# Performance work log

Hardware: AMD Instinct MI355X
Metric: run time of the kernel (lower is better)

The kernel has to match this reference:

```python
import jax, jax.numpy as jnp
import numpy as np

B, S, D, H = 32, 512, 1024, 16
DH = D // H
EPS = 1e-5
NEG = -1e9


def layer_norm(x, g, b):
    mu = jnp.mean(x, axis=-1, keepdims=True)
    var = jnp.mean(jnp.square(x - mu), axis=-1, keepdims=True)
    return (x - mu) * jax.lax.rsqrt(var + EPS) * g + b


def setup_inputs() -> dict:
    key = jax.random.key(0)
    ks = jax.random.split(key, 12)
    s = 1.0 / np.sqrt(D)
    inp = {
        "qk": jax.random.normal(ks[0], (B, S, D), jnp.float32),
        "v": jax.random.normal(ks[1], (B, S, D), jnp.float32),
        "mask": jax.random.randint(ks[2], (B, S), 0, 2).astype(jnp.int32),
        "qk_ln_g": jnp.ones((D,), jnp.float32),
        "qk_ln_b": jnp.zeros((D,), jnp.float32),
        "v_ln_g": jnp.ones((D,), jnp.float32),
        "v_ln_b": jnp.zeros((D,), jnp.float32),
        "Wq": jax.random.normal(ks[3], (D, D), jnp.float32) * s,
        "bq": jnp.zeros((D,), jnp.float32),
        "Wk": jax.random.normal(ks[4], (D, D), jnp.float32) * s,
        "bk": jnp.zeros((D,), jnp.float32),
        "Wv": jax.random.normal(ks[5], (D, D), jnp.float32) * s,
        "bv": jnp.zeros((D,), jnp.float32),
        "Wo": jax.random.normal(ks[6], (D, D), jnp.float32) * s,
        "bo": jnp.zeros((D,), jnp.float32),
    }
    return inp


def reference(qk, v, mask, qk_ln_g, qk_ln_b, v_ln_g, v_ln_b,
              Wq, bq, Wk, bk, Wv, bv, Wo, bo):
    # dual pre-norm
    qk_n = layer_norm(qk, qk_ln_g, qk_ln_b)          # [B,S,D]
    v_n = layer_norm(v, v_ln_g, v_ln_b)              # [B,S,D]
    # projections -> [B,S,H,DH]
    q = (qk_n @ Wq + bq).reshape(B, S, H, DH)
    k = (qk_n @ Wk + bk).reshape(B, S, H, DH)
    vv = (v_n @ Wv + bv).reshape(B, S, H, DH)
    # attention scores with key-padding mask
    scores = jnp.einsum("bqhd,bkhd->bhqk", q, k) / np.sqrt(DH)
    scores = jnp.where(mask[:, None, None, :] == 0, NEG, scores)
    attn = jax.nn.softmax(scores, axis=-1)           # [B,H,Sq,Sk]
    ctx = jnp.einsum("bhqk,bkhd->bqhd", attn, vv).reshape(B, S, D)
    a = ctx @ Wo + bo                                # output projection
    # residual on the normalized v (dropout is identity at eval)
    return v_n + a
```

## Files before the change

### kernel.cpp

```cpp
#include <hip/hip_runtime.h>
#include <hip/hip_bf16.h>

typedef __bf16 bf16;
typedef __bf16 bf16x2 __attribute__((ext_vector_type(2)));
typedef __bf16 bf16x4 __attribute__((ext_vector_type(4)));
typedef __bf16 bf16x8 __attribute__((ext_vector_type(8)));
typedef float f32x4 __attribute__((ext_vector_type(4)));

#define B_ 32
#define S_ 512
#define D_ 1024
#define H_ 16
#define DH_ 64
#define M_ (B_*S_)

#if __has_builtin(__builtin_amdgcn_exp2f)
#define FEXP2 __builtin_amdgcn_exp2f
#else
#define FEXP2 exp2f
#endif

__device__ __forceinline__ void async16(const void* g, void* l) {
  __builtin_amdgcn_global_load_lds(
      (const __attribute__((address_space(1))) unsigned int*)g,
      (__attribute__((address_space(3))) unsigned int*)l, 16, 0, 0);
}

__global__ __launch_bounds__(256) void ln_bf16(
    const float* __restrict__ qk, const float* __restrict__ v,
    const float* __restrict__ g1, const float* __restrict__ b1,
    const float* __restrict__ g2, const float* __restrict__ b2,
    bf16* __restrict__ o1, bf16* __restrict__ o2)
{
  int row = blockIdx.x;
  const float* src; const float* g; const float* b; bf16* o; int r;
  if (row < M_) { src=qk; g=g1; b=b1; o=o1; r=row; }
  else          { src=v;  g=g2; b=b2; o=o2; r=row-M_; }
  int t = threadIdx.x;
  float4 x = ((const float4*)(src + (size_t)r*D_))[t];
  float s  = x.x+x.y+x.z+x.w;
  float ss = x.x*x.x + x.y*x.y + x.z*x.z + x.w*x.w;
  #pragma unroll
  for (int off=32; off>=1; off>>=1) {
    s  += __shfl_xor(s,  off, 64);
    ss += __shfl_xor(ss, off, 64);
  }
  __shared__ float red[8];
  int w = t>>6, l = t&63;
  if (l==0){ red[w]=s; red[4+w]=ss; }
  __syncthreads();
  s  = red[0]+red[1]+red[2]+red[3];
  ss = red[4]+red[5]+red[6]+red[7];
  float mu  = s*(1.f/D_);
  float var = ss*(1.f/D_) - mu*mu;
  float rs  = rsqrtf(var + 1e-5f);
  float4 gg = ((const float4*)g)[t];
  float4 bb = ((const float4*)b)[t];
  bf16x4 ov;
  ov[0] = (bf16)((x.x-mu)*rs*gg.x + bb.x);
  ov[1] = (bf16)((x.y-mu)*rs*gg.y + bb.y);
  ov[2] = (bf16)((x.z-mu)*rs*gg.z + bb.z);
  ov[3] = (bf16)((x.w-mu)*rs*gg.w + bb.w);
  ((bf16x4*)(o + (size_t)r*D_))[t] = ov;
}

__global__ void wtrans(const float* __restrict__ W0, const float* __restrict__ W1,
                       const float* __restrict__ W2, const float* __restrict__ W3,
                       bf16* __restrict__ o0, bf16* __restrict__ o1,
                       bf16* __restrict__ o2, bf16* __restrict__ o3)
{
  int z = blockIdx.z;
  const float* W = z==0?W0: z==1?W1: z==2?W2: W3;
  bf16* o        = z==0?o0: z==1?o1: z==2?o2: o3;
  __shared__ float tile[32][33];
  int n0 = blockIdx.x*32, k0 = blockIdx.y*32;
  int tx = threadIdx.x, ty = threadIdx.y;
  #pragma unroll
  for (int i=0;i<4;i++) tile[ty + i*8][tx] = W[(size_t)(k0+ty+i*8)*D_ + n0+tx];
  __syncthreads();
  #pragma unroll
  for (int i=0;i<4;i++) o[(size_t)(n0+ty+i*8)*D_ + k0+tx] = (bf16)tile[tx][ty+i*8];
}

template<int MODE>
__global__ __launch_bounds__(256) void gemm_bt(
    const bf16* __restrict__ A, const bf16* __restrict__ Bt,
    const float* __restrict__ bias0, const float* __restrict__ bias1,
    const bf16* __restrict__ res,
    bf16* __restrict__ out0, bf16* __restrict__ out1, float* __restrict__ outf)
{
  __shared__ bf16 A_sh[2][128*64];
  __shared__ bf16 B_sh[2][128*64];
  int t = threadIdx.x;
  int nwg  = gridDim.x * gridDim.y;
  int orig = blockIdx.y * gridDim.x + blockIdx.x;
  int qch  = nwg >> 3;
  int wg   = (orig & 7) * qch + (orig >> 3);
  int bx = wg % gridDim.x, by = wg / gridDim.x;
  int n0 = bx*128, m0 = by*128;
  int w = t>>6, l = t&63, lr = l&15, lg = (l>>4)&3;
  int wm = w>>1, wn = w&1;

  auto stage = [&](int buf, int kt){
    const bf16* Ab = A  + (size_t)m0*D_ + kt*64;
    const bf16* Bb = Bt + (size_t)n0*D_ + kt*64;
    #pragma unroll
    for (int i=0;i<4;i++){
      int c = i*256 + t;
      int row = c>>3, slot = (c&7) ^ (row&7);
      async16(Ab + (size_t)row*D_ + slot*8, &A_sh[buf][c*8]);
      async16(Bb + (size_t)row*D_ + slot*8, &B_sh[buf][c*8]);
    }
  };

  f32x4 acc[4][4];
  #pragma unroll
  for (int m=0;m<4;m++)
    #pragma unroll
    for (int n=0;n<4;n++) acc[m][n] = (f32x4){0.f,0.f,0.f,0.f};

  stage(0, 0);
  stage(1, 1);
  asm volatile("s_waitcnt vmcnt(8)" ::: "memory");
  __builtin_amdgcn_s_barrier();

  for (int kt=0; kt<16; ++kt) {
    int cur = kt & 1;
    bf16x8 af[4][2], bfr[4][2];
    #pragma unroll
    for (int m=0;m<4;m++){
      int row = wm*64 + m*16 + lr;
      #pragma unroll
      for (int kk=0;kk<2;kk++)
        af[m][kk] = *(const bf16x8*)&A_sh[cur][row*64 + (((kk*4+lg)^(lr&7))*8)];
    }
    #pragma unroll
    for (int n=0;n<4;n++){
      int row = wn*64 + n*16 + lr;
      #pragma unroll
      for (int kk=0;kk<2;kk++)
        bfr[n][kk] = *(const bf16x8*)&B_sh[cur][row*64 + (((kk*4+lg)^(lr&7))*8)];
    }
    asm volatile("s_waitcnt lgkmcnt(0)" ::: "memory");
    __builtin_amdgcn_sched_barrier(0);
    __builtin_amdgcn_s_barrier();
    if (kt+2 < 16) stage(cur, kt+2);
    __builtin_amdgcn_s_setprio(1);
    #pragma unroll
    for (int kk=0;kk<2;kk++)
      #pragma unroll
      for (int m=0;m<4;m++)
        #pragma unroll
        for (int n=0;n<4;n++)
          acc[m][n] = __builtin_amdgcn_mfma_f32_16x16x32_bf16(af[m][kk], bfr[n][kk], acc[m][n], 0,0,0);
    __builtin_amdgcn_s_setprio(0);
    if (kt < 14)       asm volatile("s_waitcnt vmcnt(8)" ::: "memory");
    else if (kt == 14) asm volatile("s_waitcnt vmcnt(0)" ::: "memory");
    if (kt < 15) { __builtin_amdgcn_sched_barrier(0); __builtin_amdgcn_s_barrier(); }
  }

  if (MODE == 0) {
    #pragma unroll
    for (int n=0;n<4;n++){
      int col = n0 + wn*64 + n*16 + lr;
      bf16* dst; int c;
      if (col < D_) { dst = out0; c = col; } else { dst = out1; c = col - D_; }
      float bv = (col < D_) ? bias0[c] : bias1[c];
      #pragma unroll
      for (int m=0;m<4;m++){
        #pragma unroll
        for (int j=0;j<4;j++){
          size_t row = (size_t)m0 + wm*64 + m*16 + lg*4 + j;
          dst[row*D_ + c] = (bf16)(acc[m][n][j] + bv);
        }
      }
    }
  } else if (MODE == 1) {
    #pragma unroll
    for (int n=0;n<4;n++){
      int col = n0 + wn*64 + n*16 + lr;
      int hh = col >> 6, dh = col & 63;
      int nd = dh >> 4, lrk = dh & 15;
      float bv = bias0[col];
      #pragma unroll
      for (int m=0;m<4;m++){
        int row = m0 + wm*64 + m*16 + lg*4;
        int bb = row >> 9, sl = row & 511;
        int kt = sl >> 6, l0 = sl & 63;
        int kk = (l0>>5)&1, h8 = (l0>>4)&1, lgk = (l0>>2)&3;
        int c  = ((nd*2+kk)*4+lgk)*16 + lrk;
        bf16x4 pk4;
        #pragma unroll
        for (int j=0;j<4;j++) pk4[j] = (bf16)(acc[m][n][j] + bv);
        *(bf16x4*)&out0[(size_t)(((bb*H_ + hh)*8 + kt)*4096) + c*8 + h8*4] = pk4;
      }
    }
  } else {
    #pragma unroll
    for (int m=0;m<4;m++){
      #pragma unroll
      for (int j=0;j<4;j++){
        size_t row = (size_t)m0 + wm*64 + m*16 + lg*4 + j;
        #pragma unroll
        for (int n=0;n<4;n++){
          int col = n0 + wn*64 + n*16 + lr;
          size_t idx = row*D_ + col;
          outf[idx] = acc[m][n][j] + bias0[col] + (float)res[idx];
        }
      }
    }
  }
}

__global__ __launch_bounds__(512) void attn_fwd(
    const bf16* __restrict__ Q, const bf16* __restrict__ K,
    const bf16* __restrict__ VF, const int* __restrict__ mask,
    bf16* __restrict__ ctx)
{
  int flat = blockIdx.x + (blockIdx.y<<1) + (blockIdx.z<<5);
  int work = (flat & 7)*128 + (flat >> 3);
  int qt = work & 1, h = (work>>1) & 15, b = work >> 5;
  int q0 = qt*256;
  int t = threadIdx.x, w = t>>6, l = t&63, lr = l&15, lg = (l>>4)&3;

  __shared__ bf16 K_s[2][4096];
  __shared__ bf16 V_s[2][4096];
  __shared__ float msk[512];

  const float SC = 0.125f * 1.44269504f;
  msk[t] = mask[b*S_+t] ? 0.f : -1.44269504e9f;

  size_t qbase  = ((size_t)(b*S_ + q0)*H_ + h)*DH_;
  size_t vfbase = (size_t)(b*H_ + h)*8*4096;

  auto stageKV = [&](int slot, int kt){
    size_t kb = ((size_t)(b*S_ + kt*64)*H_ + h)*DH_;
    int clr=t&15, clg=(t>>4)&3, ckk=(t>>6)&1, n16=t>>7;
    async16(K + kb + (size_t)(n16*16+clr)*D_ + ckk*32 + clg*8, &K_s[slot][t*8]);
    async16(VF + vfbase + (size_t)kt*4096 + t*8, &V_s[slot][t*8]);
  };

  bf16x8 qa[2][2];
  #pragma unroll
  for (int s=0;s<2;s++)
    #pragma unroll
    for (int kk=0;kk<2;kk++)
      qa[s][kk] = *(const bf16x8*)(Q + qbase + (size_t)(w*32 + s*16 + lr)*D_ + kk*32 + lg*8);

  stageKV(0, 0);
  stageKV(1, 1);
  asm volatile("s_waitcnt vmcnt(2) lgkmcnt(0)" ::: "memory");
  __builtin_amdgcn_s_barrier();

  f32x4 cacc[2][4];
  #pragma unroll
  for (int s=0;s<2;s++)
    #pragma unroll
    for (int n=0;n<4;n++) cacc[s][n] = (f32x4){0.f,0.f,0.f,0.f};
  float mrun[2] = {-3.0e38f, -3.0e38f};
  float lrun[2] = {0.f, 0.f};

  union UPA { unsigned u[4]; bf16x8 v; };
  UPA pa[2][2];

  for (int kt=0; kt<8; ++kt) {
    int cur = kt & 1;
    const bf16* Ks = K_s[cur];
    const bf16* Vs = V_s[cur];

    bf16x8 kf[4][2];
    #pragma unroll
    for (int n=0;n<4;n++)
      #pragma unroll
      for (int kk=0;kk<2;kk++)
        kf[n][kk] = *(const bf16x8*)&Ks[(((n*2+kk)*4+lg)*16+lr)*8];

    #pragma unroll
    for (int s=0;s<2;s++){
      float p[4][4];
      #pragma unroll
      for (int n=0;n<4;n++){
        f32x4 sa = (f32x4){0.f,0.f,0.f,0.f};
        #pragma unroll
        for (int kk=0;kk<2;kk++)
          sa = __builtin_amdgcn_mfma_f32_16x16x32_bf16(kf[n][kk], qa[s][kk], sa, 0,0,0);
        float4 mk = *(const float4*)&msk[kt*64 + n*16 + lg*4];
        p[n][0] = sa[0]*SC + mk.x;
        p[n][1] = sa[1]*SC + mk.y;
        p[n][2] = sa[2]*SC + mk.z;
        p[n][3] = sa[3]*SC + mk.w;
      }

      float pm = fmaxf(fmaxf(p[0][0],p[0][1]),fmaxf(p[0][2],p[0][3]));
      #pragma unroll
      for (int n=1;n<4;n++)
        pm = fmaxf(pm, fmaxf(fmaxf(p[n][0],p[n][1]),fmaxf(p[n][2],p[n][3])));
      pm = fmaxf(pm, __shfl_xor(pm, 16, 64));
      pm = fmaxf(pm, __shfl_xor(pm, 32, 64));

      if (__any((int)(pm - mrun[s] > 8.f))) {
        float mnew  = fmaxf(mrun[s], pm);
        float alpha = FEXP2(mrun[s] - mnew);
        mrun[s] = mnew;
        lrun[s] *= alpha;
        #pragma unroll
        for (int n=0;n<4;n++) cacc[s][n] *= alpha;
      }
      float ps = 0.f;
      #pragma unroll
      for (int n=0;n<4;n++)
        #pragma unroll
        for (int j=0;j<4;j++){ p[n][j] = FEXP2(p[n][j] - mrun[s]); ps += p[n][j]; }
      ps += __shfl_xor(ps, 16, 64);
      ps += __shfl_xor(ps, 32, 64);
      lrun[s] += ps;

      unsigned pk[4][2];
      #pragma unroll
      for (int n=0;n<4;n++)
        #pragma unroll
        for (int i=0;i<2;i++){
          union { bf16x2 v; unsigned u; } u2;
          u2.v[0] = (bf16)p[n][2*i];
          u2.v[1] = (bf16)p[n][2*i+1];
          pk[n][i] = u2.u;
        }
      #pragma unroll
      for (int kk=0;kk<2;kk++){
        pa[s][kk].u[0] = pk[2*kk  ][0];
        pa[s][kk].u[1] = pk[2*kk  ][1];
        pa[s][kk].u[2] = pk[2*kk+1][0];
        pa[s][kk].u[3] = pk[2*kk+1][1];
      }
    }

    __builtin_amdgcn_s_setprio(1);
    #pragma unroll
    for (int nd=0;nd<4;nd++){
      bf16x8 vb0 = *(const bf16x8*)&Vs[(((nd*2+0)*4+lg)*16+lr)*8];
      bf16x8 vb1 = *(const bf16x8*)&Vs[(((nd*2+1)*4+lg)*16+lr)*8];
      #pragma unroll
      for (int s=0;s<2;s++){
        cacc[s][nd] = __builtin_amdgcn_mfma_f32_16x16x32_bf16(vb0, pa[s][0].v, cacc[s][nd], 0,0,0);
        cacc[s][nd] = __builtin_amdgcn_mfma_f32_16x16x32_bf16(vb1, pa[s][1].v, cacc[s][nd], 0,0,0);
      }
    }
    __builtin_amdgcn_s_setprio(0);

    asm volatile("s_waitcnt lgkmcnt(0)" ::: "memory");
    __builtin_amdgcn_sched_barrier(0);
    __builtin_amdgcn_s_barrier();
    if (kt+2 < 8) stageKV(cur, kt+2);

    if (kt < 6)       asm volatile("s_waitcnt vmcnt(2)" ::: "memory");
    else if (kt == 6) asm volatile("s_waitcnt vmcnt(0)" ::: "memory");
    if (kt < 7) { __builtin_amdgcn_sched_barrier(0); __builtin_amdgcn_s_barrier(); }
  }

  #pragma unroll
  for (int s=0;s<2;s++){
    float rl = 1.0f / lrun[s];
    size_t obase = qbase + (size_t)(w*32 + s*16 + lr)*D_;
    #pragma unroll
    for (int nd=0;nd<4;nd++){
      bf16x4 o4;
      #pragma unroll
      for (int j=0;j<4;j++) o4[j] = (bf16)(cacc[s][nd][j]*rl);
      *(bf16x4*)&ctx[obase + nd*16 + lg*4] = o4;
    }
  }
}

extern "C" void kernel_launch(void* const* d_in, const int* in_sizes, int n_in,
                              void* d_out, int out_size, void* d_ws, size_t ws_size,
                              hipStream_t stream)
{
  (void)in_sizes; (void)n_in; (void)out_size; (void)ws_size;
  const float* qk   = (const float*)d_in[0];
  const float* v    = (const float*)d_in[1];
  const int*   mask = (const int*)  d_in[2];
  const float* qk_g = (const float*)d_in[3];
  const float* qk_b = (const float*)d_in[4];
  const float* v_g  = (const float*)d_in[5];
  const float* v_b  = (const float*)d_in[6];
  const float* Wq   = (const float*)d_in[7];
  const float* bq   = (const float*)d_in[8];
  const float* Wk   = (const float*)d_in[9];
  const float* bk   = (const float*)d_in[10];
  const float* Wv   = (const float*)d_in[11];
  const float* bv   = (const float*)d_in[12];
  const float* Wo   = (const float*)d_in[13];
  const float* bo   = (const float*)d_in[14];
  float* out = (float*)d_out;

  char* ws = (char*)d_ws;
  size_t off = 0;
  auto alloc = [&](size_t bytes){ void* p = ws + off; off += (bytes + 255) & ~(size_t)255; return p; };
  bf16* qkn  = (bf16*)alloc((size_t)M_*D_*2);
  bf16* vn   = (bf16*)alloc((size_t)M_*D_*2);
  bf16* Qb   = (bf16*)alloc((size_t)M_*D_*2);
  bf16* Kb   = (bf16*)alloc((size_t)M_*D_*2);
  bf16* VFb  = (bf16*)alloc((size_t)M_*D_*2);
  bf16* Cb   = (bf16*)alloc((size_t)M_*D_*2);
  bf16* WqkT = (bf16*)alloc((size_t)2*D_*D_*2);
  bf16* WvT  = (bf16*)alloc((size_t)D_*D_*2);
  bf16* WoT  = (bf16*)alloc((size_t)D_*D_*2);

  ln_bf16<<<2*M_, 256, 0, stream>>>(qk, v, qk_g, qk_b, v_g, v_b, qkn, vn);
  wtrans<<<dim3(32,32,4), dim3(32,8), 0, stream>>>(Wq, Wk, Wv, Wo,
      WqkT, WqkT + (size_t)D_*D_, WvT, WoT);
  gemm_bt<0><<<dim3(16,128), 256, 0, stream>>>(qkn, WqkT, bq, bk, nullptr, Qb, Kb, nullptr);
  gemm_bt<1><<<dim3(8,128),  256, 0, stream>>>(vn,  WvT,  bv, nullptr, nullptr, VFb, nullptr, nullptr);
  attn_fwd<<<dim3(2, 16, 32), 512, 0, stream>>>(Qb, Kb, VFb, mask, Cb);
  gemm_bt<2><<<dim3(8,128),  256, 0, stream>>>(Cb, WoT, bo, nullptr, vn, nullptr, nullptr, out);
}
```

Measured before the change: 257.4 us.

## Load K and V fragments directly from global memory in attention kernel

Removes the double-buffered LDS staging of K and V tiles, along with its async copies, waitcnts and barriers. Each wave now reads its K and V MFMA fragments straight from global memory, relying on the caches to serve the reuse across the eight waves. This drops the synchronisation and LDS traffic and frees LDS for occupancy. In exchange, global/L2 traffic rises, and the loads are no longer prefetched ahead of the compute, so latency becomes exposed.

```diff
diff --git a/kernel.cpp b/kernel.cpp
--- a/kernel.cpp
+++ b/kernel.cpp
@@ -223,22 +223,13 @@
   int q0 = qt*256;
   int t = threadIdx.x, w = t>>6, l = t&63, lr = l&15, lg = (l>>4)&3;
 
-  __shared__ bf16 K_s[2][4096];
-  __shared__ bf16 V_s[2][4096];
   __shared__ float msk[512];
-
   const float SC = 0.125f * 1.44269504f;
   msk[t] = mask[b*S_+t] ? 0.f : -1.44269504e9f;
 
   size_t qbase  = ((size_t)(b*S_ + q0)*H_ + h)*DH_;
+  size_t kbase  = ((size_t)(b*S_)*H_ + h)*DH_;
   size_t vfbase = (size_t)(b*H_ + h)*8*4096;
-
-  auto stageKV = [&](int slot, int kt){
-    size_t kb = ((size_t)(b*S_ + kt*64)*H_ + h)*DH_;
-    int clr=t&15, clg=(t>>4)&3, ckk=(t>>6)&1, n16=t>>7;
-    async16(K + kb + (size_t)(n16*16+clr)*D_ + ckk*32 + clg*8, &K_s[slot][t*8]);
-    async16(VF + vfbase + (size_t)kt*4096 + t*8, &V_s[slot][t*8]);
-  };
 
   bf16x8 qa[2][2];
   #pragma unroll
@@ -247,10 +238,7 @@
     for (int kk=0;kk<2;kk++)
       qa[s][kk] = *(const bf16x8*)(Q + qbase + (size_t)(w*32 + s*16 + lr)*D_ + kk*32 + lg*8);
 
-  stageKV(0, 0);
-  stageKV(1, 1);
-  asm volatile("s_waitcnt vmcnt(2) lgkmcnt(0)" ::: "memory");
-  __builtin_amdgcn_s_barrier();
+  __syncthreads();
 
   f32x4 cacc[2][4];
   #pragma unroll
@@ -264,16 +252,15 @@
   UPA pa[2][2];
 
   for (int kt=0; kt<8; ++kt) {
-    int cur = kt & 1;
-    const bf16* Ks = K_s[cur];
-    const bf16* Vs = V_s[cur];
+    const bf16* Kt = K + kbase + (size_t)(kt*64)*D_;
+    const bf16* Vt = VF + vfbase + (size_t)kt*4096;
 
     bf16x8 kf[4][2];
     #pragma unroll
     for (int n=0;n<4;n++)
       #pragma unroll
       for (int kk=0;kk<2;kk++)
-        kf[n][kk] = *(const bf16x8*)&Ks[(((n*2+kk)*4+lg)*16+lr)*8];
+        kf[n][kk] = *(const bf16x8*)(Kt + (size_t)(n*16+lr)*D_ + kk*32 + lg*8);
 
     #pragma unroll
     for (int s=0;s<2;s++){
@@ -334,27 +321,16 @@
       }
     }
 
-    __builtin_amdgcn_s_setprio(1);
     #pragma unroll
     for (int nd=0;nd<4;nd++){
-      bf16x8 vb0 = *(const bf16x8*)&Vs[(((nd*2+0)*4+lg)*16+lr)*8];
-      bf16x8 vb1 = *(const bf16x8*)&Vs[(((nd*2+1)*4+lg)*16+lr)*8];
+      bf16x8 vb0 = *(const bf16x8*)(Vt + (((nd*2+0)*4+lg)*16+lr)*8);
+      bf16x8 vb1 = *(const bf16x8*)(Vt + (((nd*2+1)*4+lg)*16+lr)*8);
       #pragma unroll
       for (int s=0;s<2;s++){
         cacc[s][nd] = __builtin_amdgcn_mfma_f32_16x16x32_bf16(vb0, pa[s][0].v, cacc[s][nd], 0,0,0);
         cacc[s][nd] = __builtin_amdgcn_mfma_f32_16x16x32_bf16(vb1, pa[s][1].v, cacc[s][nd], 0,0,0);
       }
     }
-    __builtin_amdgcn_s_setprio(0);
-
-    asm volatile("s_waitcnt lgkmcnt(0)" ::: "memory");
-    __builtin_amdgcn_sched_barrier(0);
-    __builtin_amdgcn_s_barrier();
-    if (kt+2 < 8) stageKV(cur, kt+2);
-
-    if (kt < 6)       asm volatile("s_waitcnt vmcnt(2)" ::: "memory");
-    else if (kt == 6) asm volatile("s_waitcnt vmcnt(0)" ::: "memory");
-    if (kt < 7) { __builtin_amdgcn_sched_barrier(0); __builtin_amdgcn_s_barrier(); }
   }
 
   #pragma unroll
```

Result: slower. 286.0 us (+11.1%).
